# Kernel tuning notes

Hardware: AMD Instinct MI355X
Metric: run time of the kernel (lower is better)

The kernel has to match this reference:

```python
import jax, jax.numpy as jnp
import numpy as np

SEQ_LEN = 2048
NUM_HEADS = 16
DIM_EMB = 1024
DIM_HEAD = DIM_EMB // NUM_HEADS  # 64
DIM_K = DIM_EMB  # source scales by dim_k**-0.5 with dim_k defaulting to dim_emb
BASE = 10000
EPS = float(np.finfo(np.float32).eps)


def _rope_tables(seq_len, dim_head):
    idx = jnp.arange(seq_len, dtype=jnp.float32)
    scale = 1.0 / (BASE ** (jnp.arange(0, dim_head, 2, dtype=jnp.float32) / dim_head) + EPS)
    pos = jnp.outer(idx, scale)              # [S, dh/2]
    pos = jnp.concatenate([pos, pos], axis=-1)  # [S, dh]
    return jnp.cos(pos), jnp.sin(pos)


def _rotate_half(x):
    x1, x2 = x[..., : DIM_HEAD // 2], x[..., DIM_HEAD // 2 :]
    return jnp.concatenate([-x2, x1], axis=-1)


def _apply_rope(x, cos, sin):
    # x: [B, H, S, dh]; cos/sin: [S, dh]
    return x * cos[None, None] + _rotate_half(x) * sin[None, None]


def setup_inputs() -> dict:
    key = jax.random.key(0)
    k1, k2, k3 = jax.random.split(key, 3)
    x = jax.random.normal(k1, (2, SEQ_LEN, DIM_EMB), dtype=jnp.float32)
    Wqkv = jax.random.normal(k2, (DIM_EMB, 3 * DIM_EMB), dtype=jnp.float32) * 0.02
    Wout = jax.random.normal(k3, (DIM_EMB, DIM_EMB), dtype=jnp.float32) * 0.02
    return {"x": x, "Wqkv": Wqkv, "Wout": Wout}


def reference(x, Wqkv, Wout):
    B = x.shape[0]
    cos, sin = _rope_tables(SEQ_LEN, DIM_HEAD)
    qkv = x @ Wqkv  # [B, S, 3*E]
    q, k, v = jnp.split(qkv, 3, axis=-1)

    def to_heads(t):
        return t.reshape(B, SEQ_LEN, NUM_HEADS, DIM_HEAD).transpose(0, 2, 1, 3)

    q, k, v = to_heads(q), to_heads(k), to_heads(v)
    q = _apply_rope(q, cos, sin)
    k = _apply_rope(k, cos, sin)

    scores = jnp.einsum('bhsd,bhtd->bhst', q, k) * (DIM_K ** -0.5)
    causal_mask = jnp.triu(jnp.ones((SEQ_LEN, SEQ_LEN), dtype=bool), k=1)
    scores = jnp.where(causal_mask[None, None], -jnp.inf, scores)
    attn = jax.nn.softmax(scores, axis=-1)
    out = jnp.einsum('bhst,bhtd->bhsd', attn, v)
    out = out.transpose(0, 2, 1, 3).reshape(B, SEQ_LEN, DIM_EMB)
    return out @ Wout
```

## Files before the change

### kernel.cpp

```cpp
#include <hip/hip_runtime.h>

#define S_LEN 2048
#define NHEAD 16

using f32x4  = __attribute__((ext_vector_type(4))) float;
using f32x16 = __attribute__((ext_vector_type(16))) float;
using bf16x8 = __attribute__((ext_vector_type(8))) __bf16;

__device__ __forceinline__ unsigned short f2bf(float f) {
  union { float f; unsigned u; } v; v.f = f;
  unsigned r = v.u + 0x7FFFu + ((v.u >> 16) & 1u);
  return (unsigned short)(r >> 16);
}
__device__ __forceinline__ float bf2f(unsigned short h) {
  union { unsigned u; float f; } v; v.u = ((unsigned)h) << 16; return v.f;
}
__device__ __forceinline__ void unpack8(uint4 u, float x[8]) {
  x[0]=bf2f((unsigned short)(u.x&0xffff)); x[1]=bf2f((unsigned short)(u.x>>16));
  x[2]=bf2f((unsigned short)(u.y&0xffff)); x[3]=bf2f((unsigned short)(u.y>>16));
  x[4]=bf2f((unsigned short)(u.z&0xffff)); x[5]=bf2f((unsigned short)(u.z>>16));
  x[6]=bf2f((unsigned short)(u.w&0xffff)); x[7]=bf2f((unsigned short)(u.w>>16));
}
__device__ __forceinline__ uint4 pack8(const unsigned short o[8]) {
  uint4 u;
  u.x = (unsigned)o[0] | ((unsigned)o[1]<<16);
  u.y = (unsigned)o[2] | ((unsigned)o[3]<<16);
  u.z = (unsigned)o[4] | ((unsigned)o[5]<<16);
  u.w = (unsigned)o[6] | ((unsigned)o[7]<<16);
  return u;
}
__device__ __forceinline__ void gload16(const void* g, void* l) {
  __builtin_amdgcn_global_load_lds(
      (const __attribute__((address_space(1))) unsigned int*)g,
      (__attribute__((address_space(3))) unsigned int*)l, 16, 0, 0);
}
__device__ __forceinline__ float exp2_fast(float x) {
#if __has_builtin(__builtin_amdgcn_exp2f)
  return __builtin_amdgcn_exp2f(x);
#else
  return __expf(x * 0.6931471805599453f);
#endif
}
__device__ __forceinline__ void store_c(float* C, size_t off, float v) { C[off] = v; }
__device__ __forceinline__ void store_c(unsigned short* C, size_t off, float v) { C[off] = f2bf(v); }

__global__ __launch_bounds__(256) void k_cvt(const float* __restrict__ in,
                                             unsigned short* __restrict__ out, int n8) {
  int i = blockIdx.x * 256 + threadIdx.x;
  if (i >= n8) return;
  const float4* p = (const float4*)in + 2 * (size_t)i;
  float4 a = p[0], b = p[1];
  unsigned short o[8] = { f2bf(a.x), f2bf(a.y), f2bf(a.z), f2bf(a.w),
                          f2bf(b.x), f2bf(b.y), f2bf(b.z), f2bf(b.w) };
  ((uint4*)out)[i] = pack8(o);
}

__global__ __launch_bounds__(256) void k_transpose_cvt(const float* __restrict__ in,
                                                       unsigned short* __restrict__ out,
                                                       int R, int C) {
  __shared__ float T[64][65];
  int r0 = blockIdx.x * 64, c0 = blockIdx.y * 64;
  int tid = threadIdx.x;
#pragma unroll
  for (int i = 0; i < 16; ++i) {
    int idx = tid + i * 256;
    int r = idx >> 6, c = idx & 63;
    T[r][c] = in[(size_t)(r0 + r) * C + c0 + c];
  }
  __syncthreads();
#pragma unroll
  for (int i = 0; i < 8; ++i) {
    int idx = tid + i * 256;
    int co = idx >> 5, rp = (idx & 31) * 2;
    unsigned v = (unsigned)f2bf(T[rp][co]) | ((unsigned)f2bf(T[rp + 1][co]) << 16);
    *(unsigned*)&out[(size_t)(c0 + co) * R + r0 + rp] = v;
  }
}

template <typename OUT_T>
__global__ __launch_bounds__(256, 2) void k_gemm128(const unsigned short* __restrict__ A,
                                                    const unsigned short* __restrict__ Bt,
                                                    OUT_T* __restrict__ C,
                                                    int M, int N, int K) {
  __shared__ unsigned short As[2][128][64];
  __shared__ unsigned short Bs[2][128][64];
  const int tid = threadIdx.x;
  const int lane = tid & 63, w = tid >> 6;
  const int wm = w >> 1, wn = w & 1;
  const int li = lane & 15, g = lane >> 4;
  const int m0 = blockIdx.x * 128, n0 = blockIdx.y * 128;
  const int srow = w * 8 + (lane >> 3);
  const int scol = ((lane & 7) ^ ((lane >> 3) & 7)) * 8;

  f32x4 acc[4][4];
#pragma unroll
  for (int i = 0; i < 4; ++i)
#pragma unroll
    for (int j = 0; j < 4; ++j) acc[i][j] = (f32x4){0.f, 0.f, 0.f, 0.f};

  const int nt = K >> 6;

  auto stage_tile = [&](int kt) {
    int buf = kt & 1;
    const unsigned short* sa = A + (size_t)(m0 + srow) * K + kt * 64 + scol;
    const unsigned short* sb = Bt + (size_t)(n0 + srow) * K + kt * 64 + scol;
    char* da = (char*)&As[buf][srow][0];
    char* db = (char*)&Bs[buf][srow][0];
#pragma unroll
    for (int j = 0; j < 4; ++j) {
      gload16(sa + (size_t)(j * 32) * K, da + j * 32 * 128);
      gload16(sb + (size_t)(j * 32) * K, db + j * 32 * 128);
    }
  };

  stage_tile(0);

  for (int i = 0; i < nt; ++i) {
    if (i + 1 < nt) {
      stage_tile(i + 1);
      asm volatile("s_waitcnt vmcnt(8)" ::: "memory");
    } else {
      asm volatile("s_waitcnt vmcnt(0)" ::: "memory");
    }
    __builtin_amdgcn_s_barrier();
    asm volatile("" ::: "memory");
    const int buf = i & 1;
#pragma unroll
    for (int kk = 0; kk < 2; ++kk) {
      bf16x8 af[4], bfv[4];
      const int ps = ((kk << 2) | g) ^ (li & 7);
#pragma unroll
      for (int ii = 0; ii < 4; ++ii)
        af[ii] = *(const bf16x8*)&As[buf][wm * 64 + ii * 16 + li][ps * 8];
#pragma unroll
      for (int jj = 0; jj < 4; ++jj)
        bfv[jj] = *(const bf16x8*)&Bs[buf][wn * 64 + jj * 16 + li][ps * 8];
      __builtin_amdgcn_s_setprio(1);
#pragma unroll
      for (int ii = 0; ii < 4; ++ii)
#pragma unroll
        for (int jj = 0; jj < 4; ++jj)
          acc[ii][jj] = __builtin_amdgcn_mfma_f32_16x16x32_bf16(af[ii], bfv[jj],
                                                                acc[ii][jj], 0, 0, 0);
      __builtin_amdgcn_s_setprio(0);
    }
    asm volatile("" ::: "memory");
    __builtin_amdgcn_s_barrier();
    asm volatile("" ::: "memory");
  }

#pragma unroll
  for (int ii = 0; ii < 4; ++ii) {
    int row = m0 + wm * 64 + ii * 16 + g * 4;
#pragma unroll
    for (int jj = 0; jj < 4; ++jj) {
      int col = n0 + wn * 64 + jj * 16 + li;
#pragma unroll
      for (int r = 0; r < 4; ++r) store_c(C, (size_t)(row + r) * N + col, acc[ii][jj][r]);
    }
  }
}

__global__ __launch_bounds__(256) void k_rope_split(const unsigned short* __restrict__ qkv,
                                                    unsigned short* __restrict__ Qf,
                                                    unsigned short* __restrict__ Kf,
                                                    unsigned short* __restrict__ Vf) {
  int blk = blockIdx.x;
  int st = blk & 31, h = (blk >> 5) & 15, b = blk >> 9;
  int s0 = st * 64;
  int tid = threadIdx.x;
  int sl = tid >> 2, quad = tid & 3;
  int s = s0 + sl;
  int bh = b * NHEAD + h;
  int l31 = s & 31;
  int qt = s >> 5;
  int cq = quad >> 1, hiq = quad & 1;

  float cs[8], sn[8];
#pragma unroll
  for (int j = 0; j < 8; ++j) {
    int pr = quad * 8 + j;
    float e2 = exp2_fast((float)pr * 0.41524101f);
    float freq = 1.0f / (e2 + 1.1920928955078125e-07f);
    float x = (float)s * freq * 0.15915494309189535f;
    x -= floorf(x);
    float ang = x * 6.283185307179586f;
    sn[j] = __sinf(ang);
    cs[j] = __cosf(ang);
  }
  const unsigned short* row = qkv + (size_t)(b * S_LEN + s) * 3072;
  const float QSC = 0.04508422f;
  {
    float x1[8], x2[8];
    unpack8(*(const uint4*)&row[h * 64 + quad * 8], x1);
    unpack8(*(const uint4*)&row[h * 64 + 32 + quad * 8], x2);
    unsigned short o1[8], o2[8];
#pragma unroll
    for (int j = 0; j < 8; ++j) {
      o1[j] = f2bf((x1[j] * cs[j] - x2[j] * sn[j]) * QSC);
      o2[j] = f2bf((x2[j] * cs[j] + x1[j] * sn[j]) * QSC);
    }
    size_t base = ((size_t)bh * 64 + qt) * 4;
    int lane8 = (hiq * 32 + l31) * 8;
    *(uint4*)&Qf[(base + cq) * 512 + lane8] = pack8(o1);
    *(uint4*)&Qf[(base + 2 + cq) * 512 + lane8] = pack8(o2);
  }
  {
    float x1[8], x2[8];
    unpack8(*(const uint4*)&row[1024 + h * 64 + quad * 8], x1);
    unpack8(*(const uint4*)&row[1024 + h * 64 + 32 + quad * 8], x2);
    unsigned short o1[8], o2[8];
#pragma unroll
    for (int j = 0; j < 8; ++j) {
      o1[j] = f2bf(x1[j] * cs[j] - x2[j] * sn[j]);
      o2[j] = f2bf(x2[j] * cs[j] + x1[j] * sn[j]);
    }
    int lp = (l31 & 0x13) | ((l31 & 4) << 1) | ((l31 & 8) >> 1);
    size_t base = ((size_t)bh * 64 + qt) * 4;
    int lane8 = (hiq * 32 + lp) * 8;
    *(uint4*)&Kf[(base + cq) * 512 + lane8] = pack8(o1);
    *(uint4*)&Kf[(base + 2 + cq) * 512 + lane8] = pack8(o2);
  }
  __shared__ unsigned short Vl[64 * 72];
#pragma unroll
  for (int i = 0; i < 2; ++i) {
    int c = tid + i * 256;
    int r = c >> 3, c8 = (c & 7) * 8;
    *(uint4*)&Vl[r * 72 + c8] =
        *(const uint4*)&qkv[(size_t)(b * S_LEN + s0 + r) * 3072 + 2048 + h * 64 + c8];
  }
  __syncthreads();
  int d = tid >> 2, sc4 = tid & 3;
  unsigned o[8];
#pragma unroll
  for (int jj = 0; jj < 8; ++jj) {
    int sidx = sc4 * 16 + jj * 2;
    o[jj] = (unsigned)Vl[sidx * 72 + d] | ((unsigned)Vl[(sidx + 1) * 72 + d] << 16);
  }
  {
    int t = st * 2 + (sc4 >> 1);
    int c = ((d >> 5) << 1) + (sc4 & 1);
    size_t base = (((size_t)bh * 64 + t) * 4 + c) * 512;
    *(uint4*)&Vf[base + (d & 31) * 8]        = make_uint4(o[0], o[1], o[2], o[3]);
    *(uint4*)&Vf[base + (32 + (d & 31)) * 8] = make_uint4(o[4], o[5], o[6], o[7]);
  }
}

__global__ __launch_bounds__(256) void k_attn4(const unsigned short* __restrict__ Qf,
                                               const unsigned short* __restrict__ Kf,
                                               const unsigned short* __restrict__ Vf,
                                               unsigned short* __restrict__ O) {
  __shared__ float MBUF[3][2176];
  int bid = blockIdx.x;
  int i = (bid & 7) * 256 + (bid >> 3);
  int bh = i >> 6;
  int qt = 63 - (i & 63);
  int tid = threadIdx.x, w = tid >> 6, lane = tid & 63;
  int b = bh >> 4, h = bh & 15;
  int l31 = lane & 31, hi = lane >> 5;

  int n = qt + 1;
  int t0 = (w * n) >> 2, t1 = ((w + 1) * n) >> 2;

  const unsigned short* Kg = Kf + ((size_t)bh * 64) * 4 * 512 + lane * 8;
  const unsigned short* Vg = Vf + ((size_t)bh * 64) * 4 * 512 + lane * 8;

  float m_run = -1e30f, l_run = 0.f;
  f32x16 acc0, acc1;
#pragma unroll
  for (int r = 0; r < 16; ++r) { acc0[r] = 0.f; acc1[r] = 0.f; }

  if (t0 < t1) {
    const unsigned short* Qg = Qf + (((size_t)bh * 64 + qt) * 4) * 512 + lane * 8;
    bf16x8 qf[4];
#pragma unroll
    for (int c = 0; c < 4; ++c) qf[c] = *(const bf16x8*)(Qg + c * 512);

    auto loadK = [&](bf16x8 (&kf)[4], int t) {
      const unsigned short* kp = Kg + (size_t)t * 2048;
#pragma unroll
      for (int c = 0; c < 4; ++c) kf[c] = *(const bf16x8*)(kp + c * 512);
    };
    auto loadV = [&](bf16x8 (&vf)[4], int t) {
      const unsigned short* vp = Vg + (size_t)t * 2048;
#pragma unroll
      for (int c = 0; c < 4; ++c) vf[c] = *(const bf16x8*)(vp + c * 512);
    };
    auto step = [&](bf16x8 (&kf)[4], bf16x8 (&vf)[4], int t) {
      f32x16 s;
#pragma unroll
      for (int r = 0; r < 16; ++r) s[r] = 0.f;
      __builtin_amdgcn_s_setprio(1);
      s = __builtin_amdgcn_mfma_f32_32x32x16_bf16(kf[0], qf[0], s, 0, 0, 0);
      s = __builtin_amdgcn_mfma_f32_32x32x16_bf16(kf[1], qf[1], s, 0, 0, 0);
      s = __builtin_amdgcn_mfma_f32_32x32x16_bf16(kf[2], qf[2], s, 0, 0, 0);
      s = __builtin_amdgcn_mfma_f32_32x32x16_bf16(kf[3], qf[3], s, 0, 0, 0);
      __builtin_amdgcn_s_setprio(0);
      if (t == qt) {
#pragma unroll
        for (int r = 0; r < 16; ++r) {
          int kv = (r & 7) + 16 * (r >> 3) + 8 * hi;
          if (kv > l31) s[r] = -1e30f;
        }
      }
      float pmax;
      {
        float m0 = fmaxf(s[0], s[1]),   mm1 = fmaxf(s[2], s[3]);
        float m2 = fmaxf(s[4], s[5]),   m3 = fmaxf(s[6], s[7]);
        float m4 = fmaxf(s[8], s[9]),   m5 = fmaxf(s[10], s[11]);
        float m6 = fmaxf(s[12], s[13]), m7 = fmaxf(s[14], s[15]);
        m0 = fmaxf(m0, mm1); m2 = fmaxf(m2, m3); m4 = fmaxf(m4, m5); m6 = fmaxf(m6, m7);
        pmax = fmaxf(fmaxf(m0, m2), fmaxf(m4, m6));
      }
      if (__any(pmax > m_run + 8.0f)) {
        float pfull = fmaxf(pmax, __shfl_xor(pmax, 32));
        float mnew = fmaxf(m_run, pfull);
        float fac = exp2_fast(m_run - mnew);
        l_run *= fac;
#pragma unroll
        for (int r = 0; r < 16; ++r) { acc0[r] *= fac; acc1[r] *= fac; }
        m_run = mnew;
      }
#pragma unroll
      for (int r = 0; r < 16; ++r) s[r] = exp2_fast(s[r] - m_run);
      {
        float s0 = (s[0] + s[1]) + (s[2] + s[3]);
        float s1 = (s[4] + s[5]) + (s[6] + s[7]);
        float s2 = (s[8] + s[9]) + (s[10] + s[11]);
        float s3 = (s[12] + s[13]) + (s[14] + s[15]);
        l_run += (s0 + s1) + (s2 + s3);
      }
      bf16x8 pf0, pf1;
      {
        unsigned w0, w1, w2, w3;
        asm("v_cvt_pk_bf16_f32 %0, %1, %2" : "=v"(w0) : "v"(s[0]), "v"(s[1]));
        asm("v_cvt_pk_bf16_f32 %0, %1, %2" : "=v"(w1) : "v"(s[2]), "v"(s[3]));
        asm("v_cvt_pk_bf16_f32 %0, %1, %2" : "=v"(w2) : "v"(s[4]), "v"(s[5]));
        asm("v_cvt_pk_bf16_f32 %0, %1, %2" : "=v"(w3) : "v"(s[6]), "v"(s[7]));
        union { uint4 uu; bf16x8 v; } cv;
        cv.uu = make_uint4(w0, w1, w2, w3);
        pf0 = cv.v;
        asm("v_cvt_pk_bf16_f32 %0, %1, %2" : "=v"(w0) : "v"(s[8]), "v"(s[9]));
        asm("v_cvt_pk_bf16_f32 %0, %1, %2" : "=v"(w1) : "v"(s[10]), "v"(s[11]));
        asm("v_cvt_pk_bf16_f32 %0, %1, %2" : "=v"(w2) : "v"(s[12]), "v"(s[13]));
        asm("v_cvt_pk_bf16_f32 %0, %1, %2" : "=v"(w3) : "v"(s[14]), "v"(s[15]));
        cv.uu = make_uint4(w0, w1, w2, w3);
        pf1 = cv.v;
      }
      __builtin_amdgcn_s_setprio(1);
      acc0 = __builtin_amdgcn_mfma_f32_32x32x16_bf16(vf[0], pf0, acc0, 0, 0, 0);
      acc0 = __builtin_amdgcn_mfma_f32_32x32x16_bf16(vf[1], pf1, acc0, 0, 0, 0);
      acc1 = __builtin_amdgcn_mfma_f32_32x32x16_bf16(vf[2], pf0, acc1, 0, 0, 0);
      acc1 = __builtin_amdgcn_mfma_f32_32x32x16_bf16(vf[3], pf1, acc1, 0, 0, 0);
      __builtin_amdgcn_s_setprio(0);
    };

    bf16x8 kA[4], vA[4], kB[4], vB[4];
    loadK(kA, t0); loadV(vA, t0);
    int t = t0;
    while (true) {
      if (t + 1 < t1) { loadK(kB, t + 1); loadV(vB, t + 1); }
      step(kA, vA, t);
      ++t; if (t >= t1) break;
      if (t + 1 < t1) { loadK(kA, t + 1); loadV(vA, t + 1); }
      step(kB, vB, t);
      ++t; if (t >= t1) break;
    }
  }

  if (w != 0) {
    float* sb = &MBUF[w - 1][0];
#pragma unroll
    for (int r = 0; r < 16; ++r) {
      sb[r * 64 + lane] = acc0[r];
      sb[(16 + r) * 64 + lane] = acc1[r];
    }
    sb[2048 + lane] = m_run;
    sb[2112 + lane] = l_run;
  }
  __syncthreads();
  if (w == 0) {
    float m1 = MBUF[0][2048 + lane], m2 = MBUF[1][2048 + lane], m3 = MBUF[2][2048 + lane];
    float mF = fmaxf(fmaxf(m_run, m1), fmaxf(m2, m3));
    float f0 = exp2_fast(m_run - mF);
    float f1 = exp2_fast(m1 - mF);
    float f2 = exp2_fast(m2 - mF);
    float f3 = exp2_fast(m3 - mF);
    float lF = f0 * l_run + f1 * MBUF[0][2112 + lane] + f2 * MBUF[1][2112 + lane] +
               f3 * MBUF[2][2112 + lane];
    lF += __shfl_xor(lF, 32);
    float inv = 1.0f / lF;
    f32x16 o0, o1;
#pragma unroll
    for (int r = 0; r < 16; ++r) {
      o0[r] = (f0 * acc0[r] + f1 * MBUF[0][r * 64 + lane] + f2 * MBUF[1][r * 64 + lane] +
               f3 * MBUF[2][r * 64 + lane]) * inv;
      o1[r] = (f0 * acc1[r] + f1 * MBUF[0][(16 + r) * 64 + lane] +
               f2 * MBUF[1][(16 + r) * 64 + lane] + f3 * MBUF[2][(16 + r) * 64 + lane]) * inv;
    }
    unsigned short* ol = (unsigned short*)&MBUF[0][0];
#pragma unroll
    for (int dh = 0; dh < 2; ++dh) {
#pragma unroll
      for (int r = 0; r < 16; r += 2) {
        int dv = dh * 32 + (r & 3) + 8 * (r >> 2) + 4 * hi;
        float lo = dh ? o1[r] : o0[r];
        float hi_ = dh ? o1[r + 1] : o0[r + 1];
        unsigned uu;
        asm("v_cvt_pk_bf16_f32 %0, %1, %2" : "=v"(uu) : "v"(lo), "v"(hi_));
        *(unsigned*)&ol[l31 * 72 + dv] = uu;
      }
    }
    asm volatile("s_waitcnt lgkmcnt(0)" ::: "memory");
    int q0f = qt * 32;
    int q = lane >> 1, half = lane & 1;
    unsigned short* op = O + ((size_t)(b * S_LEN + q0f + q)) * 1024 + h * 64 + half * 32;
#pragma unroll
    for (int j = 0; j < 4; ++j)
      *(uint4*)(op + j * 8) = *(const uint4*)&ol[q * 72 + half * 32 + j * 8];
  }
}

extern "C" void kernel_launch(void* const* d_in, const int* in_sizes, int n_in,
                              void* d_out, int out_size, void* d_ws, size_t ws_size,
                              hipStream_t stream) {
  const float* x = (const float*)d_in[0];
  const float* Wqkv = (const float*)d_in[1];
  const float* Wout = (const float*)d_in[2];
  float* out = (float*)d_out;
  char* ws = (char*)d_ws;
  unsigned short* xb = (unsigned short*)(ws);
  unsigned short* WqkvT = (unsigned short*)(ws + ((size_t)8 << 20));
  unsigned short* WoutT = (unsigned short*)(ws + ((size_t)14 << 20));
  unsigned short* qkv = (unsigned short*)(ws + ((size_t)16 << 20));
  unsigned short* Qf = (unsigned short*)(ws + ((size_t)40 << 20));
  unsigned short* Kf = (unsigned short*)(ws + ((size_t)48 << 20));
  unsigned short* Vf = (unsigned short*)(ws + ((size_t)56 << 20));

  k_cvt<<<2048, 256, 0, stream>>>(x, xb, 4096 * 1024 / 8);
  k_transpose_cvt<<<dim3(16, 48), 256, 0, stream>>>(Wqkv, WqkvT, 1024, 3072);
  k_transpose_cvt<<<dim3(16, 16), 256, 0, stream>>>(Wout, WoutT, 1024, 1024);
  k_gemm128<unsigned short><<<dim3(32, 24), 256, 0, stream>>>(xb, WqkvT, qkv, 4096, 3072, 1024);
  k_rope_split<<<1024, 256, 0, stream>>>(qkv, Qf, Kf, Vf);
  k_attn4<<<2048, 256, 0, stream>>>(Qf, Kf, Vf, xb );
  k_gemm128<float><<<dim3(32, 8), 256, 0, stream>>>(xb, WoutT, out, 4096, 1024, 1024);
}
```

Measured before the change: 121.9 us.

## Process two KV tiles per iteration in attention with interleaved MFMAs

Restructures the attention inner loop to handle two 32-key tiles at once. The QK^T MFMAs of both tiles are interleaved, one shared max and rescale check is done per pair, and the PV MFMAs are chained. K and V prefetches for the next pair are issued right after their respective MFMA phases, and an odd leftover tile goes through a single-tile tail. This is meant to hide MFMA dependency latency and halve the per-tile softmax bookkeeping, at the cost of higher register pressure.

```diff
diff --git a/kernel.cpp b/kernel.cpp
--- a/kernel.cpp
+++ b/kernel.cpp
@@ -246,7 +246,7 @@
   }
 }
 
-__global__ __launch_bounds__(256) void k_attn4(const unsigned short* __restrict__ Qf,
+__global__ __launch_bounds__(256) void k_attn5(const unsigned short* __restrict__ Qf,
                                                const unsigned short* __restrict__ Kf,
                                                const unsigned short* __restrict__ Vf,
                                                unsigned short* __restrict__ O) {
@@ -286,15 +286,115 @@
 #pragma unroll
       for (int c = 0; c < 4; ++c) vf[c] = *(const bf16x8*)(vp + c * 512);
     };
-    auto step = [&](bf16x8 (&kf)[4], bf16x8 (&vf)[4], int t) {
+    auto rescale_check = [&](float pmax) {
+      if (__any(pmax > m_run + 8.0f)) {
+        float pfull = fmaxf(pmax, __shfl_xor(pmax, 32));
+        float mnew = fmaxf(m_run, pfull);
+        float fac = exp2_fast(m_run - mnew);
+        l_run *= fac;
+#pragma unroll
+        for (int r = 0; r < 16; ++r) { acc0[r] *= fac; acc1[r] *= fac; }
+        m_run = mnew;
+      }
+    };
+    auto cvt2 = [&](const f32x16& s, bf16x8& p0, bf16x8& p1) {
+      unsigned w0, w1, w2, w3;
+      asm("v_cvt_pk_bf16_f32 %0, %1, %2" : "=v"(w0) : "v"(s[0]), "v"(s[1]));
+      asm("v_cvt_pk_bf16_f32 %0, %1, %2" : "=v"(w1) : "v"(s[2]), "v"(s[3]));
+      asm("v_cvt_pk_bf16_f32 %0, %1, %2" : "=v"(w2) : "v"(s[4]), "v"(s[5]));
+      asm("v_cvt_pk_bf16_f32 %0, %1, %2" : "=v"(w3) : "v"(s[6]), "v"(s[7]));
+      union { uint4 uu; bf16x8 v; } cv;
+      cv.uu = make_uint4(w0, w1, w2, w3);
+      p0 = cv.v;
+      asm("v_cvt_pk_bf16_f32 %0, %1, %2" : "=v"(w0) : "v"(s[8]), "v"(s[9]));
+      asm("v_cvt_pk_bf16_f32 %0, %1, %2" : "=v"(w1) : "v"(s[10]), "v"(s[11]));
+      asm("v_cvt_pk_bf16_f32 %0, %1, %2" : "=v"(w2) : "v"(s[12]), "v"(s[13]));
+      asm("v_cvt_pk_bf16_f32 %0, %1, %2" : "=v"(w3) : "v"(s[14]), "v"(s[15]));
+      cv.uu = make_uint4(w0, w1, w2, w3);
+      p1 = cv.v;
+    };
+
+    bf16x8 kA[4], vA[4], kB[4], vB[4];
+    loadK(kA, t0); loadV(vA, t0);
+    if (t0 + 1 < t1) { loadK(kB, t0 + 1); loadV(vB, t0 + 1); }
+    int t = t0;
+    while (t + 1 < t1) {
+      int tb = t + 1;
+      f32x16 sa, sb;
+#pragma unroll
+      for (int r = 0; r < 16; ++r) { sa[r] = 0.f; sb[r] = 0.f; }
+      __builtin_amdgcn_s_setprio(1);
+      sa = __builtin_amdgcn_mfma_f32_32x32x16_bf16(kA[0], qf[0], sa, 0, 0, 0);
+      sb = __builtin_amdgcn_mfma_f32_32x32x16_bf16(kB[0], qf[0], sb, 0, 0, 0);
+      sa = __builtin_amdgcn_mfma_f32_32x32x16_bf16(kA[1], qf[1], sa, 0, 0, 0);
+      sb = __builtin_amdgcn_mfma_f32_32x32x16_bf16(kB[1], qf[1], sb, 0, 0, 0);
+      sa = __builtin_amdgcn_mfma_f32_32x32x16_bf16(kA[2], qf[2], sa, 0, 0, 0);
+      sb = __builtin_amdgcn_mfma_f32_32x32x16_bf16(kB[2], qf[2], sb, 0, 0, 0);
+      sa = __builtin_amdgcn_mfma_f32_32x32x16_bf16(kA[3], qf[3], sa, 0, 0, 0);
+      sb = __builtin_amdgcn_mfma_f32_32x32x16_bf16(kB[3], qf[3], sb, 0, 0, 0);
+      __builtin_amdgcn_s_setprio(0);
+      if (t + 2 < t1) loadK(kA, t + 2);
+      if (t + 3 < t1) loadK(kB, t + 3);
+      if (tb == qt) {
+#pragma unroll
+        for (int r = 0; r < 16; ++r) {
+          int kv = (r & 7) + 16 * (r >> 3) + 8 * hi;
+          if (kv > l31) sb[r] = -1e30f;
+        }
+      }
+      float pmax;
+      {
+        float m[8];
+#pragma unroll
+        for (int r = 0; r < 8; ++r)
+          m[r] = fmaxf(fmaxf(sa[2 * r], sa[2 * r + 1]), fmaxf(sb[2 * r], sb[2 * r + 1]));
+        m[0] = fmaxf(m[0], m[1]); m[2] = fmaxf(m[2], m[3]);
+        m[4] = fmaxf(m[4], m[5]); m[6] = fmaxf(m[6], m[7]);
+        pmax = fmaxf(fmaxf(m[0], m[2]), fmaxf(m[4], m[6]));
+      }
+      rescale_check(pmax);
+#pragma unroll
+      for (int r = 0; r < 16; ++r) {
+        sa[r] = exp2_fast(sa[r] - m_run);
+        sb[r] = exp2_fast(sb[r] - m_run);
+      }
+      {
+        float t0_ = 0.f, t1_ = 0.f, t2_ = 0.f, t3_ = 0.f;
+#pragma unroll
+        for (int r = 0; r < 4; ++r) {
+          t0_ += sa[r] + sb[r];
+          t1_ += sa[4 + r] + sb[4 + r];
+          t2_ += sa[8 + r] + sb[8 + r];
+          t3_ += sa[12 + r] + sb[12 + r];
+        }
+        l_run += (t0_ + t1_) + (t2_ + t3_);
+      }
+      bf16x8 pa0, pa1, pb0, pb1;
+      cvt2(sa, pa0, pa1);
+      cvt2(sb, pb0, pb1);
+      __builtin_amdgcn_s_setprio(1);
+      acc0 = __builtin_amdgcn_mfma_f32_32x32x16_bf16(vA[0], pa0, acc0, 0, 0, 0);
+      acc1 = __builtin_amdgcn_mfma_f32_32x32x16_bf16(vA[2], pa0, acc1, 0, 0, 0);
+      acc0 = __builtin_amdgcn_mfma_f32_32x32x16_bf16(vA[1], pa1, acc0, 0, 0, 0);
+      acc1 = __builtin_amdgcn_mfma_f32_32x32x16_bf16(vA[3], pa1, acc1, 0, 0, 0);
+      acc0 = __builtin_amdgcn_mfma_f32_32x32x16_bf16(vB[0], pb0, acc0, 0, 0, 0);
+      acc1 = __builtin_amdgcn_mfma_f32_32x32x16_bf16(vB[2], pb0, acc1, 0, 0, 0);
+      acc0 = __builtin_amdgcn_mfma_f32_32x32x16_bf16(vB[1], pb1, acc0, 0, 0, 0);
+      acc1 = __builtin_amdgcn_mfma_f32_32x32x16_bf16(vB[3], pb1, acc1, 0, 0, 0);
+      __builtin_amdgcn_s_setprio(0);
+      if (t + 2 < t1) loadV(vA, t + 2);
+      if (t + 3 < t1) loadV(vB, t + 3);
+      t += 2;
+    }
+    if (t < t1) {
       f32x16 s;
 #pragma unroll
       for (int r = 0; r < 16; ++r) s[r] = 0.f;
       __builtin_amdgcn_s_setprio(1);
-      s = __builtin_amdgcn_mfma_f32_32x32x16_bf16(kf[0], qf[0], s, 0, 0, 0);
-      s = __builtin_amdgcn_mfma_f32_32x32x16_bf16(kf[1], qf[1], s, 0, 0, 0);
-      s = __builtin_amdgcn_mfma_f32_32x32x16_bf16(kf[2], qf[2], s, 0, 0, 0);
-      s = __builtin_amdgcn_mfma_f32_32x32x16_bf16(kf[3], qf[3], s, 0, 0, 0);
+      s = __builtin_amdgcn_mfma_f32_32x32x16_bf16(kA[0], qf[0], s, 0, 0, 0);
+      s = __builtin_amdgcn_mfma_f32_32x32x16_bf16(kA[1], qf[1], s, 0, 0, 0);
+      s = __builtin_amdgcn_mfma_f32_32x32x16_bf16(kA[2], qf[2], s, 0, 0, 0);
+      s = __builtin_amdgcn_mfma_f32_32x32x16_bf16(kA[3], qf[3], s, 0, 0, 0);
       __builtin_amdgcn_s_setprio(0);
       if (t == qt) {
 #pragma unroll
@@ -312,15 +412,7 @@
         m0 = fmaxf(m0, mm1); m2 = fmaxf(m2, m3); m4 = fmaxf(m4, m5); m6 = fmaxf(m6, m7);
         pmax = fmaxf(fmaxf(m0, m2), fmaxf(m4, m6));
       }
-      if (__any(pmax > m_run + 8.0f)) {
-        float pfull = fmaxf(pmax, __shfl_xor(pmax, 32));
-        float mnew = fmaxf(m_run, pfull);
-        float fac = exp2_fast(m_run - mnew);
-        l_run *= fac;
-#pragma unroll
-        for (int r = 0; r < 16; ++r) { acc0[r] *= fac; acc1[r] *= fac; }
-        m_run = mnew;
-      }
+      rescale_check(pmax);
 #pragma unroll
       for (int r = 0; r < 16; ++r) s[r] = exp2_fast(s[r] - m_run);
       {
@@ -331,40 +423,13 @@
         l_run += (s0 + s1) + (s2 + s3);
       }
       bf16x8 pf0, pf1;
-      {
-        unsigned w0, w1, w2, w3;
-        asm("v_cvt_pk_bf16_f32 %0, %1, %2" : "=v"(w0) : "v"(s[0]), "v"(s[1]));
-        asm("v_cvt_pk_bf16_f32 %0, %1, %2" : "=v"(w1) : "v"(s[2]), "v"(s[3]));
-        asm("v_cvt_pk_bf16_f32 %0, %1, %2" : "=v"(w2) : "v"(s[4]), "v"(s[5]));
-        asm("v_cvt_pk_bf16_f32 %0, %1, %2" : "=v"(w3) : "v"(s[6]), "v"(s[7]));
-        union { uint4 uu; bf16x8 v; } cv;
-        cv.uu = make_uint4(w0, w1, w2, w3);
-        pf0 = cv.v;
-        asm("v_cvt_pk_bf16_f32 %0, %1, %2" : "=v"(w0) : "v"(s[8]), "v"(s[9]));
-        asm("v_cvt_pk_bf16_f32 %0, %1, %2" : "=v"(w1) : "v"(s[10]), "v"(s[11]));
-        asm("v_cvt_pk_bf16_f32 %0, %1, %2" : "=v"(w2) : "v"(s[12]), "v"(s[13]));
-        asm("v_cvt_pk_bf16_f32 %0, %1, %2" : "=v"(w3) : "v"(s[14]), "v"(s[15]));
-        cv.uu = make_uint4(w0, w1, w2, w3);
-        pf1 = cv.v;
-      }
+      cvt2(s, pf0, pf1);
       __builtin_amdgcn_s_setprio(1);
-      acc0 = __builtin_amdgcn_mfma_f32_32x32x16_bf16(vf[0], pf0, acc0, 0, 0, 0);
-      acc0 = __builtin_amdgcn_mfma_f32_32x32x16_bf16(vf[1], pf1, acc0, 0, 0, 0);
-      acc1 = __builtin_amdgcn_mfma_f32_32x32x16_bf16(vf[2], pf0, acc1, 0, 0, 0);
-      acc1 = __builtin_amdgcn_mfma_f32_32x32x16_bf16(vf[3], pf1, acc1, 0, 0, 0);
+      acc0 = __builtin_amdgcn_mfma_f32_32x32x16_bf16(vA[0], pf0, acc0, 0, 0, 0);
+      acc0 = __builtin_amdgcn_mfma_f32_32x32x16_bf16(vA[1], pf1, acc0, 0, 0, 0);
+      acc1 = __builtin_amdgcn_mfma_f32_32x32x16_bf16(vA[2], pf0, acc1, 0, 0, 0);
+      acc1 = __builtin_amdgcn_mfma_f32_32x32x16_bf16(vA[3], pf1, acc1, 0, 0, 0);
       __builtin_amdgcn_s_setprio(0);
-    };
-
-    bf16x8 kA[4], vA[4], kB[4], vB[4];
-    loadK(kA, t0); loadV(vA, t0);
-    int t = t0;
-    while (true) {
-      if (t + 1 < t1) { loadK(kB, t + 1); loadV(vB, t + 1); }
-      step(kA, vA, t);
-      ++t; if (t >= t1) break;
-      if (t + 1 < t1) { loadK(kA, t + 1); loadV(vA, t + 1); }
-      step(kB, vB, t);
-      ++t; if (t >= t1) break;
     }
   }
 
@@ -442,6 +507,6 @@
   k_transpose_cvt<<<dim3(16, 16), 256, 0, stream>>>(Wout, WoutT, 1024, 1024);
   k_gemm128<unsigned short><<<dim3(32, 24), 256, 0, stream>>>(xb, WqkvT, qkv, 4096, 3072, 1024);
   k_rope_split<<<1024, 256, 0, stream>>>(qkv, Qf, Kf, Vf);
-  k_attn4<<<2048, 256, 0, stream>>>(Qf, Kf, Vf, xb );
+  k_attn5<<<2048, 256, 0, stream>>>(Qf, Kf, Vf, xb );
   k_gemm128<float><<<dim3(32, 8), 256, 0, stream>>>(xb, WoutT, out, 4096, 1024, 1024);
 }
```

Result: no change. 120.2 us (median of 2 runs) (-1.3%).
